# Optimization experiments

Hardware: AMD Instinct MI355X
Metric: run time of the kernel (lower is better)

Reference implementation:

```python
import jax, jax.numpy as jnp
import numpy as np

CDIM = 256  # part_size for energy_pooling_mask


def setup_inputs() -> dict:
    key = jax.random.key(0)
    ks = jax.random.split(key, 6)
    B, T, IDIM, HDIM, ODIM = 8, 2048, 512, 2048, 512
    x = jax.random.normal(ks[0], (B, T, IDIM), dtype=jnp.float32)
    mask_prev = jax.random.randint(ks[1], (B, T, HDIM), 0, 2, dtype=jnp.int32)
    W_enc = jax.random.normal(ks[2], (HDIM, IDIM), dtype=jnp.float32) * 0.02
    b_enc = jax.random.normal(ks[3], (HDIM,), dtype=jnp.float32) * 0.02
    W_dec = jax.random.normal(ks[4], (ODIM, HDIM), dtype=jnp.float32) * 0.02
    b_dec = jax.random.normal(ks[5], (ODIM,), dtype=jnp.float32) * 0.02
    return {"x": x, "mask_prev": mask_prev, "W_enc": W_enc, "b_enc": b_enc,
            "W_dec": W_dec, "b_dec": b_dec}


def _energy_pooling_mask(h, part_size):
    # topk over channel (last) dim of h^2; share=True -> k = 2*part_size
    B, T, H = h.shape
    k2 = 2 * part_size
    _, idx = jax.lax.top_k(h * h, k2)            # [B, T, 2c] unique indices
    idx_f = idx.reshape(B * T, k2)
    rows = jnp.arange(B * T)[:, None]
    base = jnp.zeros((B * T, H), dtype=h.dtype)
    # sum of one-hots over unique indices == scatter-set of 1.0
    mask_share = base.at[rows, idx_f].set(1.0).reshape(B, T, H)
    mask_cur = base.at[rows, idx_f[:, :part_size]].set(1.0).reshape(B, T, H)
    return mask_cur, mask_share


def reference(x, mask_prev, W_enc, b_enc, W_dec, b_dec):
    # encoder: Linear(idim -> hdim)
    h = jnp.einsum('bti,hi->bth', x, W_enc) + b_enc
    # hidden_exclude_activation with mask_prev given:
    # h[mask_prev.bool()] = 0
    mp = mask_prev.astype(h.dtype)
    h = jnp.where(mp > 0, jnp.zeros((), h.dtype), h)
    mask_cur, mask_cur_share = _energy_pooling_mask(h, CDIM)
    mask_prev_new = mp + mask_cur
    # h.masked_fill(~mask_cur_share.bool(), 0)
    h = h * mask_cur_share
    # decoder_src: Linear(hdim -> odim)
    out = jnp.einsum('bth,oh->bto', h, W_dec) + b_dec
    return out, mask_prev_new
```

## Files before the change

### kernel.cpp

```cpp
#include <hip/hip_runtime.h>
#include <hip/hip_bf16.h>

typedef __attribute__((ext_vector_type(8))) __bf16 bf16x8;
typedef __attribute__((ext_vector_type(4))) float f32x4;

#define MDIM 16384
#define HDIM 2048
#define IDIM 512
#define ODIM 512
#define SCAP 512

static __device__ __forceinline__ unsigned short f2bf(float f) {
  unsigned int u = __float_as_uint(f);
  unsigned int r = (u + 0x7fffu + ((u >> 16) & 1u)) >> 16;
  return (unsigned short)r;
}

__global__ void cvt_bf16_kernel(const float* __restrict__ src,
                                unsigned short* __restrict__ dst, int n) {
  int i = (blockIdx.x * 256 + threadIdx.x) * 4;
  if (i >= n) return;
  float4 v = *(const float4*)(src + i);
  unsigned int a = (unsigned int)f2bf(v.x) | ((unsigned int)f2bf(v.y) << 16);
  unsigned int b = (unsigned int)f2bf(v.z) | ((unsigned int)f2bf(v.w) << 16);
  uint2 st; st.x = a; st.y = b;
  *(uint2*)(dst + i) = st;
}

__global__ __launch_bounds__(256) void gemm1_kernel(
    const float* __restrict__ x,
    const float* __restrict__ wenc,
    const float* __restrict__ benc,
    float* __restrict__ h) {
  __shared__ __align__(16) float As[32][132];
  __shared__ __align__(16) float Bs[32][132];
  const int t = threadIdx.x;
  const int tx = t & 15, ty = t >> 4;
  const int m0 = blockIdx.y * 128;
  const int n0 = blockIdx.x * 128;
  const int r0 = t >> 1;
  const int kh = (t & 1) * 16;

  const float* pa = x + (size_t)(m0 + r0) * IDIM + kh;
  const float* pb = wenc + (size_t)(n0 + r0) * IDIM + kh;

  float acc[8][8];
#pragma unroll
  for (int i = 0; i < 8; ++i)
#pragma unroll
    for (int j = 0; j < 8; ++j) acc[i][j] = 0.f;

  for (int kt = 0; kt < IDIM; kt += 32) {
    float4 a0 = *(const float4*)(pa + kt);
    float4 a1 = *(const float4*)(pa + kt + 4);
    float4 a2 = *(const float4*)(pa + kt + 8);
    float4 a3 = *(const float4*)(pa + kt + 12);
    float4 b0 = *(const float4*)(pb + kt);
    float4 b1 = *(const float4*)(pb + kt + 4);
    float4 b2 = *(const float4*)(pb + kt + 8);
    float4 b3 = *(const float4*)(pb + kt + 12);
    __syncthreads();
    {
      const float av[16] = {a0.x, a0.y, a0.z, a0.w, a1.x, a1.y, a1.z, a1.w,
                            a2.x, a2.y, a2.z, a2.w, a3.x, a3.y, a3.z, a3.w};
      const float bv[16] = {b0.x, b0.y, b0.z, b0.w, b1.x, b1.y, b1.z, b1.w,
                            b2.x, b2.y, b2.z, b2.w, b3.x, b3.y, b3.z, b3.w};
#pragma unroll
      for (int j = 0; j < 16; ++j) {
        As[kh + j][r0] = av[j];
        Bs[kh + j][r0] = bv[j];
      }
    }
    __syncthreads();
#pragma unroll
    for (int k = 0; k < 32; ++k) {
      float4 av0 = *(const float4*)&As[k][ty * 4];
      float4 av1 = *(const float4*)&As[k][64 + ty * 4];
      float4 bv0 = *(const float4*)&Bs[k][tx * 4];
      float4 bv1 = *(const float4*)&Bs[k][64 + tx * 4];
      float am[8] = {av0.x, av0.y, av0.z, av0.w, av1.x, av1.y, av1.z, av1.w};
      float bm[8] = {bv0.x, bv0.y, bv0.z, bv0.w, bv1.x, bv1.y, bv1.z, bv1.w};
#pragma unroll
      for (int i = 0; i < 8; ++i)
#pragma unroll
        for (int j = 0; j < 8; ++j) acc[i][j] += am[i] * bm[j];
    }
  }
  float4 be0 = *(const float4*)(benc + n0 + tx * 4);
  float4 be1 = *(const float4*)(benc + n0 + 64 + tx * 4);
  float bb[8] = {be0.x, be0.y, be0.z, be0.w, be1.x, be1.y, be1.z, be1.w};
#pragma unroll
  for (int i = 0; i < 8; ++i) {
    int m = m0 + ((i < 4) ? (ty * 4 + i) : (64 + ty * 4 + (i - 4)));
    float* hrow = h + (size_t)m * HDIM + n0;
    float4 s0 = {acc[i][0] + bb[0], acc[i][1] + bb[1], acc[i][2] + bb[2], acc[i][3] + bb[3]};
    float4 s1 = {acc[i][4] + bb[4], acc[i][5] + bb[5], acc[i][6] + bb[6], acc[i][7] + bb[7]};
    *(float4*)(hrow + tx * 4) = s0;
    *(float4*)(hrow + 64 + tx * 4) = s1;
  }
}

__global__ __launch_bounds__(256, 4) void select_kernel(
    float* __restrict__ hbuf,
    const int* __restrict__ maskp,
    unsigned short* __restrict__ hs) {
  const int t = threadIdx.x;
  const int lane = t & 63;
  const int w = t >> 6;
  const int row = blockIdx.x * 4 + w;

  __shared__ int hist[4][1024];
  __shared__ unsigned int cand[4][2][SCAP];
  __shared__ int nc[4][2];

  int* H = hist[w];
  float* hrow = hbuf + (size_t)row * HDIM;
  const int* mrow = maskp + (size_t)row * HDIM;
  unsigned short* hsrow = hs + (size_t)row * HDIM;

  {
    int4 z = {0, 0, 0, 0};
#pragma unroll
    for (int i = 0; i < 4; ++i) *(int4*)&H[(i * 64 + lane) * 4] = z;
  }
  if (lane == 0) { nc[w][0] = 0; nc[w][1] = 0; }

  unsigned int key[8][4];
  uint2 hvb[8];
  unsigned int mmbits = 0;
#pragma unroll
  for (int s = 0; s < 8; ++s) {
    float4 hv = *(const float4*)(hrow + (s * 64 + lane) * 4);
    int4 mv = *(const int4*)(mrow + (s * 64 + lane) * 4);
    float h0 = (mv.x > 0) ? 0.f : hv.x;
    float h1 = (mv.y > 0) ? 0.f : hv.y;
    float h2 = (mv.z > 0) ? 0.f : hv.z;
    float h3 = (mv.w > 0) ? 0.f : hv.w;
    mmbits |= ((mv.x > 0) ? 1u : 0u) << (s * 4 + 0);
    mmbits |= ((mv.y > 0) ? 1u : 0u) << (s * 4 + 1);
    mmbits |= ((mv.z > 0) ? 1u : 0u) << (s * 4 + 2);
    mmbits |= ((mv.w > 0) ? 1u : 0u) << (s * 4 + 3);
    key[s][0] = __float_as_uint(h0 * h0);
    key[s][1] = __float_as_uint(h1 * h1);
    key[s][2] = __float_as_uint(h2 * h2);
    key[s][3] = __float_as_uint(h3 * h3);
    hvb[s].x = (unsigned int)f2bf(h0) | ((unsigned int)f2bf(h1) << 16);
    hvb[s].y = (unsigned int)f2bf(h2) | ((unsigned int)f2bf(h3) << 16);
  }

#pragma unroll
  for (int s = 0; s < 8; ++s)
#pragma unroll
    for (int c = 0; c < 4; ++c)
      if (key[s][c]) atomicAdd(&H[key[s][c] >> 21], 1);

  int q[16];
#pragma unroll
  for (int i = 0; i < 16; i += 4) {
    int4 hh = *(const int4*)&H[lane * 16 + i];
    q[i] = hh.x; q[i + 1] = hh.y; q[i + 2] = hh.z; q[i + 3] = hh.w;
  }
  int ls = 0;
#pragma unroll
  for (int i = 0; i < 16; ++i) ls += q[i];
  int rs = ls;
#pragma unroll
  for (int d = 1; d < 64; d <<= 1) {
    int o = __shfl_down(rs, d, 64);
    rs += (lane + d < 64) ? o : 0;
  }
  int f512 = -1, f256 = -1;
  {
    int c = rs - ls;
#pragma unroll
    for (int i = 15; i >= 0; --i) {
      int hc = q[i];
      if (c < 512 && c + hc >= 512) f512 = ((lane * 16 + i) << 12) | (512 - c);
      if (c < 256 && c + hc >= 256) f256 = ((lane * 16 + i) << 12) | (256 - c);
      c += hc;
    }
  }
#pragma unroll
  for (int d = 1; d < 64; d <<= 1) {
    f512 = max(f512, __shfl_xor(f512, d, 64));
    f256 = max(f256, __shfl_xor(f256, d, 64));
  }
  int b512, rb512, b256, rb256;
  if (f512 < 0) { b512 = 0; rb512 = 0x40000000; } else { b512 = f512 >> 12; rb512 = f512 & 0xfff; }
  if (f256 < 0) { b256 = 0; rb256 = 0x40000000; } else { b256 = f256 >> 12; rb256 = f256 & 0xfff; }

  unsigned int* c5 = cand[w][0];
  unsigned int* c2 = cand[w][1];
#pragma unroll
  for (int s = 0; s < 8; ++s)
#pragma unroll
    for (int c = 0; c < 4; ++c) {
      unsigned int k = key[s][c];
      if (k) {
        int bin = (int)(k >> 21);
        if (bin == b512) { int p = atomicAdd(&nc[w][0], 1); if (p < SCAP) c5[p] = k; }
        if (bin == b256) { int p = atomicAdd(&nc[w][1], 1); if (p < SCAP) c2[p] = k; }
      }
    }
  int C5 = nc[w][0]; C5 = (C5 < SCAP) ? C5 : SCAP;
  int C2 = nc[w][1]; C2 = (C2 < SCAP) ? C2 : SCAP;

  const int half = lane >> 5;
  const int hl = lane & 31;
  unsigned int bb = half ? (unsigned int)b256 : (unsigned int)b512;
  int rr = half ? rb256 : rb512;
  const unsigned int* cd = half ? c2 : c5;
  int C = half ? C2 : C5;
  unsigned int v = 0;
  if (rr <= C) {
    v = bb << 21;
    for (int bit = 20; bit >= 0; --bit) {
      unsigned int cth = v | (1u << bit);
      int cnt = 0;
      for (int p = hl; p < C; p += 32) cnt += (cd[p] >= cth) ? 1 : 0;
#pragma unroll
      for (int d = 1; d < 32; d <<= 1) cnt += __shfl_xor(cnt, d, 64);
      if (cnt >= rr) v = cth;
    }
  }
  const unsigned int v512 = (unsigned int)__shfl((int)v, 0, 64);
  const unsigned int v256 = (unsigned int)__shfl((int)v, 32, 64);

  int g = 0;
#pragma unroll
  for (int s = 0; s < 8; ++s)
#pragma unroll
    for (int c = 0; c < 4; ++c) {
      g += (key[s][c] > v512) ? 1 : 0;
      g += (key[s][c] > v256) ? (1 << 16) : 0;
    }
#pragma unroll
  for (int d = 1; d < 64; d <<= 1) g += __shfl_xor(g, d, 64);
  const int rg512 = 512 - (g & 0xffff);
  const int rg256 = 256 - (g >> 16);

  int excl = 0;
#pragma unroll
  for (int s = 0; s < 8; ++s) {
    int tcnt = 0;
#pragma unroll
    for (int c = 0; c < 4; ++c) {
      tcnt += (key[s][c] == v512) ? 1 : 0;
      tcnt += (key[s][c] == v256) ? (1 << 16) : 0;
    }
    int incl = tcnt;
#pragma unroll
    for (int d = 1; d < 64; d <<= 1) {
      int o = __shfl_up(incl, d, 64);
      if (lane >= d) incl += o;
    }
    int myexcl = excl + incl - tcnt;
    int tot = __shfl(incl, 63, 64);
    int run512 = myexcl & 0xffff;
    int run256 = (myexcl >> 16) & 0xffff;
    float mpn[4];
    unsigned int hb0 = hvb[s].x, hb1 = hvb[s].y;
#pragma unroll
    for (int c = 0; c < 4; ++c) {
      unsigned int k = key[s][c];
      bool share, cur;
      if (k > v512) share = true;
      else if (k == v512) { share = (run512 < rg512); run512++; }
      else share = false;
      if (k > v256) cur = true;
      else if (k == v256) { cur = (run256 < rg256); run256++; }
      else cur = false;
      int mm = (mmbits >> (s * 4 + c)) & 1;
      mpn[c] = (float)mm + (cur ? 1.0f : 0.0f);
      if (!share) {
        if (c == 0) hb0 &= 0xffff0000u;
        if (c == 1) hb0 &= 0x0000ffffu;
        if (c == 2) hb1 &= 0xffff0000u;
        if (c == 3) hb1 &= 0x0000ffffu;
      }
    }
    float4 so = {mpn[0], mpn[1], mpn[2], mpn[3]};
    *(float4*)(hrow + (s * 64 + lane) * 4) = so;
    uint2 ho = {hb0, hb1};
    *(uint2*)(hsrow + (s * 64 + lane) * 4) = ho;
    excl += tot;
  }
}

__global__ __launch_bounds__(256) void gemm2_kernel(
    const unsigned short* __restrict__ A,
    const unsigned short* __restrict__ B,
    const float* __restrict__ bdec,
    float* __restrict__ out) {
  __shared__ __align__(16) unsigned short As[64 * 40];
  __shared__ __align__(16) unsigned short Bs[128 * 40];
  const int t = threadIdx.x;
  const int lane = t & 63;
  const int w = t >> 6;
  const int wm = w >> 1, wn = w & 1;
  const int m0 = blockIdx.y * 64;
  const int n0 = blockIdx.x * 128;
  const int r = t >> 2;
  const int k8 = (t & 3) * 8;

  f32x4 acc[2][4];
#pragma unroll
  for (int i = 0; i < 2; ++i)
#pragma unroll
    for (int j = 0; j < 4; ++j) acc[i][j] = (f32x4){0.f, 0.f, 0.f, 0.f};

  const int la = lane & 15;
  const int kq = (lane >> 4) * 8;

  const unsigned short* pa = A + (size_t)(m0 + r) * HDIM + k8;
  const unsigned short* pb0 = B + (size_t)(n0 + r) * HDIM + k8;
  const unsigned short* pb1 = B + (size_t)(n0 + 64 + r) * HDIM + k8;

  uint4 a0 = *(const uint4*)(pa);
  uint4 b0 = *(const uint4*)(pb0);
  uint4 b1 = *(const uint4*)(pb1);

  for (int kt = 0; kt < HDIM; kt += 32) {
    __syncthreads();
    *(uint4*)&As[r * 40 + k8] = a0;
    *(uint4*)&Bs[r * 40 + k8] = b0;
    *(uint4*)&Bs[(64 + r) * 40 + k8] = b1;
    __syncthreads();
    if (kt + 32 < HDIM) {
      a0 = *(const uint4*)(pa + kt + 32);
      b0 = *(const uint4*)(pb0 + kt + 32);
      b1 = *(const uint4*)(pb1 + kt + 32);
    }
    bf16x8 af[2], bg[4];
#pragma unroll
    for (int mi = 0; mi < 2; ++mi)
      af[mi] = *(const bf16x8*)&As[(wm * 32 + mi * 16 + la) * 40 + kq];
#pragma unroll
    for (int ni = 0; ni < 4; ++ni)
      bg[ni] = *(const bf16x8*)&Bs[(wn * 64 + ni * 16 + la) * 40 + kq];
#pragma unroll
    for (int mi = 0; mi < 2; ++mi)
#pragma unroll
      for (int ni = 0; ni < 4; ++ni)
        acc[mi][ni] = __builtin_amdgcn_mfma_f32_16x16x32_bf16(
            af[mi], bg[ni], acc[mi][ni], 0, 0, 0);
  }
  const int rq = (lane >> 4) * 4;
#pragma unroll
  for (int mi = 0; mi < 2; ++mi) {
#pragma unroll
    for (int ni = 0; ni < 4; ++ni) {
      int n = n0 + wn * 64 + ni * 16 + la;
      float bd = bdec[n];
#pragma unroll
      for (int rr = 0; rr < 4; ++rr) {
        int m = m0 + wm * 32 + mi * 16 + rq + rr;
        out[(size_t)m * ODIM + n] = acc[mi][ni][rr] + bd;
      }
    }
  }
}

extern "C" void kernel_launch(void* const* d_in, const int* in_sizes, int n_in,
                              void* d_out, int out_size, void* d_ws, size_t ws_size,
                              hipStream_t stream) {
  const float* x = (const float*)d_in[0];
  const int* mask_prev = (const int*)d_in[1];
  const float* W_enc = (const float*)d_in[2];
  const float* b_enc = (const float*)d_in[3];
  const float* W_dec = (const float*)d_in[4];
  const float* b_dec = (const float*)d_in[5];

  float* out = (float*)d_out;
  float* hbuf = out + (size_t)MDIM * ODIM;
  unsigned short* hs = (unsigned short*)d_ws;
  unsigned short* wdec = hs + (size_t)MDIM * HDIM;

  cvt_bf16_kernel<<<dim3((ODIM * HDIM) / (256 * 4)), dim3(256), 0, stream>>>(
      W_dec, wdec, ODIM * HDIM);
  gemm1_kernel<<<dim3(HDIM / 128, MDIM / 128), dim3(256), 0, stream>>>(
      x, W_enc, b_enc, hbuf);
  select_kernel<<<dim3(MDIM / 4), dim3(256), 0, stream>>>(hbuf, mask_prev, hs);
  gemm2_kernel<<<dim3(ODIM / 128, MDIM / 64), dim3(256), 0, stream>>>(
      hs, wdec, b_dec, out);
}
```

Baseline: 752.9 us.

## Fuse W_dec bf16 conversion into gemm2 and add tie-free fast path in select

Drops the separate kernel that converts W_dec to bf16; gemm2 now loads fp32 W_dec and packs it to bf16 while staging into shared memory, removing one launch and an intermediate buffer. In the select kernel, the first few candidate values are cached in registers for the radix-threshold search, and when the tie counts match exactly the remaining slots, a fast path replaces the per-segment prefix-scan tie-breaking. The cost is that gemm2 now reads twice the bytes for B tiles and spends extra ALU on conversion in every block, since W_dec is reconverted per M-tile.

```diff
diff --git a/kernel.cpp b/kernel.cpp
--- a/kernel.cpp
+++ b/kernel.cpp
@@ -16,15 +16,13 @@
   return (unsigned short)r;
 }
 
-__global__ void cvt_bf16_kernel(const float* __restrict__ src,
-                                unsigned short* __restrict__ dst, int n) {
-  int i = (blockIdx.x * 256 + threadIdx.x) * 4;
-  if (i >= n) return;
-  float4 v = *(const float4*)(src + i);
-  unsigned int a = (unsigned int)f2bf(v.x) | ((unsigned int)f2bf(v.y) << 16);
-  unsigned int b = (unsigned int)f2bf(v.z) | ((unsigned int)f2bf(v.w) << 16);
-  uint2 st; st.x = a; st.y = b;
-  *(uint2*)(dst + i) = st;
+static __device__ __forceinline__ uint4 pack8bf(float4 x, float4 y) {
+  uint4 o;
+  o.x = (unsigned int)f2bf(x.x) | ((unsigned int)f2bf(x.y) << 16);
+  o.y = (unsigned int)f2bf(x.z) | ((unsigned int)f2bf(x.w) << 16);
+  o.z = (unsigned int)f2bf(y.x) | ((unsigned int)f2bf(y.y) << 16);
+  o.w = (unsigned int)f2bf(y.z) | ((unsigned int)f2bf(y.w) << 16);
+  return o;
 }
 
 __global__ __launch_bounds__(256) void gemm1_kernel(
@@ -213,11 +211,16 @@
   int C = half ? C2 : C5;
   unsigned int v = 0;
   if (rr <= C) {
+    unsigned int rc0 = (hl < C) ? cd[hl] : 0u;
+    unsigned int rc1 = (hl + 32 < C) ? cd[hl + 32] : 0u;
+    unsigned int rc2 = (hl + 64 < C) ? cd[hl + 64] : 0u;
+    unsigned int rc3 = (hl + 96 < C) ? cd[hl + 96] : 0u;
     v = bb << 21;
     for (int bit = 20; bit >= 0; --bit) {
       unsigned int cth = v | (1u << bit);
-      int cnt = 0;
-      for (int p = hl; p < C; p += 32) cnt += (cd[p] >= cth) ? 1 : 0;
+      int cnt = ((rc0 >= cth) ? 1 : 0) + ((rc1 >= cth) ? 1 : 0) +
+                ((rc2 >= cth) ? 1 : 0) + ((rc3 >= cth) ? 1 : 0);
+      for (int p = hl + 128; p < C; p += 32) cnt += (cd[p] >= cth) ? 1 : 0;
 #pragma unroll
       for (int d = 1; d < 32; d <<= 1) cnt += __shfl_xor(cnt, d, 64);
       if (cnt >= rr) v = cth;
@@ -226,70 +229,103 @@
   const unsigned int v512 = (unsigned int)__shfl((int)v, 0, 64);
   const unsigned int v256 = (unsigned int)__shfl((int)v, 32, 64);
 
-  int g = 0;
+  int g = 0, e = 0;
 #pragma unroll
   for (int s = 0; s < 8; ++s)
 #pragma unroll
     for (int c = 0; c < 4; ++c) {
       g += (key[s][c] > v512) ? 1 : 0;
       g += (key[s][c] > v256) ? (1 << 16) : 0;
-    }
-#pragma unroll
-  for (int d = 1; d < 64; d <<= 1) g += __shfl_xor(g, d, 64);
+      e += (key[s][c] == v512) ? 1 : 0;
+      e += (key[s][c] == v256) ? (1 << 16) : 0;
+    }
+#pragma unroll
+  for (int d = 1; d < 64; d <<= 1) {
+    g += __shfl_xor(g, d, 64);
+    e += __shfl_xor(e, d, 64);
+  }
   const int rg512 = 512 - (g & 0xffff);
   const int rg256 = 256 - (g >> 16);
-
-  int excl = 0;
-#pragma unroll
-  for (int s = 0; s < 8; ++s) {
-    int tcnt = 0;
-#pragma unroll
-    for (int c = 0; c < 4; ++c) {
-      tcnt += (key[s][c] == v512) ? 1 : 0;
-      tcnt += (key[s][c] == v256) ? (1 << 16) : 0;
-    }
-    int incl = tcnt;
-#pragma unroll
-    for (int d = 1; d < 64; d <<= 1) {
-      int o = __shfl_up(incl, d, 64);
-      if (lane >= d) incl += o;
-    }
-    int myexcl = excl + incl - tcnt;
-    int tot = __shfl(incl, 63, 64);
-    int run512 = myexcl & 0xffff;
-    int run256 = (myexcl >> 16) & 0xffff;
-    float mpn[4];
-    unsigned int hb0 = hvb[s].x, hb1 = hvb[s].y;
-#pragma unroll
-    for (int c = 0; c < 4; ++c) {
-      unsigned int k = key[s][c];
-      bool share, cur;
-      if (k > v512) share = true;
-      else if (k == v512) { share = (run512 < rg512); run512++; }
-      else share = false;
-      if (k > v256) cur = true;
-      else if (k == v256) { cur = (run256 < rg256); run256++; }
-      else cur = false;
-      int mm = (mmbits >> (s * 4 + c)) & 1;
-      mpn[c] = (float)mm + (cur ? 1.0f : 0.0f);
-      if (!share) {
-        if (c == 0) hb0 &= 0xffff0000u;
-        if (c == 1) hb0 &= 0x0000ffffu;
-        if (c == 2) hb1 &= 0xffff0000u;
-        if (c == 3) hb1 &= 0x0000ffffu;
-      }
-    }
-    float4 so = {mpn[0], mpn[1], mpn[2], mpn[3]};
-    *(float4*)(hrow + (s * 64 + lane) * 4) = so;
-    uint2 ho = {hb0, hb1};
-    *(uint2*)(hsrow + (s * 64 + lane) * 4) = ho;
-    excl += tot;
+  const int e512 = e & 0xffff;
+  const int e256 = e >> 16;
+
+  if (e512 == rg512 && e256 == rg256) {
+#pragma unroll
+    for (int s = 0; s < 8; ++s) {
+      float mpn[4];
+      unsigned int hb0 = hvb[s].x, hb1 = hvb[s].y;
+#pragma unroll
+      for (int c = 0; c < 4; ++c) {
+        unsigned int k = key[s][c];
+        bool share = (k >= v512);
+        bool cur = (k >= v256);
+        int mm = (mmbits >> (s * 4 + c)) & 1;
+        mpn[c] = (float)mm + (cur ? 1.0f : 0.0f);
+        if (!share) {
+          if (c == 0) hb0 &= 0xffff0000u;
+          if (c == 1) hb0 &= 0x0000ffffu;
+          if (c == 2) hb1 &= 0xffff0000u;
+          if (c == 3) hb1 &= 0x0000ffffu;
+        }
+      }
+      float4 so = {mpn[0], mpn[1], mpn[2], mpn[3]};
+      *(float4*)(hrow + (s * 64 + lane) * 4) = so;
+      uint2 ho = {hb0, hb1};
+      *(uint2*)(hsrow + (s * 64 + lane) * 4) = ho;
+    }
+  } else {
+    int excl = 0;
+#pragma unroll
+    for (int s = 0; s < 8; ++s) {
+      int tcnt = 0;
+#pragma unroll
+      for (int c = 0; c < 4; ++c) {
+        tcnt += (key[s][c] == v512) ? 1 : 0;
+        tcnt += (key[s][c] == v256) ? (1 << 16) : 0;
+      }
+      int incl = tcnt;
+#pragma unroll
+      for (int d = 1; d < 64; d <<= 1) {
+        int o = __shfl_up(incl, d, 64);
+        if (lane >= d) incl += o;
+      }
+      int myexcl = excl + incl - tcnt;
+      int tot = __shfl(incl, 63, 64);
+      int run512 = myexcl & 0xffff;
+      int run256 = (myexcl >> 16) & 0xffff;
+      float mpn[4];
+      unsigned int hb0 = hvb[s].x, hb1 = hvb[s].y;
+#pragma unroll
+      for (int c = 0; c < 4; ++c) {
+        unsigned int k = key[s][c];
+        bool share, cur;
+        if (k > v512) share = true;
+        else if (k == v512) { share = (run512 < rg512); run512++; }
+        else share = false;
+        if (k > v256) cur = true;
+        else if (k == v256) { cur = (run256 < rg256); run256++; }
+        else cur = false;
+        int mm = (mmbits >> (s * 4 + c)) & 1;
+        mpn[c] = (float)mm + (cur ? 1.0f : 0.0f);
+        if (!share) {
+          if (c == 0) hb0 &= 0xffff0000u;
+          if (c == 1) hb0 &= 0x0000ffffu;
+          if (c == 2) hb1 &= 0xffff0000u;
+          if (c == 3) hb1 &= 0x0000ffffu;
+        }
+      }
+      float4 so = {mpn[0], mpn[1], mpn[2], mpn[3]};
+      *(float4*)(hrow + (s * 64 + lane) * 4) = so;
+      uint2 ho = {hb0, hb1};
+      *(uint2*)(hsrow + (s * 64 + lane) * 4) = ho;
+      excl += tot;
+    }
   }
 }
 
 __global__ __launch_bounds__(256) void gemm2_kernel(
     const unsigned short* __restrict__ A,
-    const unsigned short* __restrict__ B,
+    const float* __restrict__ Wd,
     const float* __restrict__ bdec,
     float* __restrict__ out) {
   __shared__ __align__(16) unsigned short As[64 * 40];
@@ -313,23 +349,27 @@
   const int kq = (lane >> 4) * 8;
 
   const unsigned short* pa = A + (size_t)(m0 + r) * HDIM + k8;
-  const unsigned short* pb0 = B + (size_t)(n0 + r) * HDIM + k8;
-  const unsigned short* pb1 = B + (size_t)(n0 + 64 + r) * HDIM + k8;
+  const float* pb0 = Wd + (size_t)(n0 + r) * HDIM + k8;
+  const float* pb1 = Wd + (size_t)(n0 + 64 + r) * HDIM + k8;
 
   uint4 a0 = *(const uint4*)(pa);
-  uint4 b0 = *(const uint4*)(pb0);
-  uint4 b1 = *(const uint4*)(pb1);
+  float4 b0a = *(const float4*)(pb0);
+  float4 b0b = *(const float4*)(pb0 + 4);
+  float4 b1a = *(const float4*)(pb1);
+  float4 b1b = *(const float4*)(pb1 + 4);
 
   for (int kt = 0; kt < HDIM; kt += 32) {
     __syncthreads();
     *(uint4*)&As[r * 40 + k8] = a0;
-    *(uint4*)&Bs[r * 40 + k8] = b0;
-    *(uint4*)&Bs[(64 + r) * 40 + k8] = b1;
+    *(uint4*)&Bs[r * 40 + k8] = pack8bf(b0a, b0b);
+    *(uint4*)&Bs[(64 + r) * 40 + k8] = pack8bf(b1a, b1b);
     __syncthreads();
     if (kt + 32 < HDIM) {
       a0 = *(const uint4*)(pa + kt + 32);
-      b0 = *(const uint4*)(pb0 + kt + 32);
-      b1 = *(const uint4*)(pb1 + kt + 32);
+      b0a = *(const float4*)(pb0 + kt + 32);
+      b0b = *(const float4*)(pb0 + kt + 36);
+      b1a = *(const float4*)(pb1 + kt + 32);
+      b1b = *(const float4*)(pb1 + kt + 36);
     }
     bf16x8 af[2], bg[4];
 #pragma unroll
@@ -374,13 +414,10 @@
   float* out = (float*)d_out;
   float* hbuf = out + (size_t)MDIM * ODIM;
   unsigned short* hs = (unsigned short*)d_ws;
-  unsigned short* wdec = hs + (size_t)MDIM * HDIM;
-
-  cvt_bf16_kernel<<<dim3((ODIM * HDIM) / (256 * 4)), dim3(256), 0, stream>>>(
-      W_dec, wdec, ODIM * HDIM);
+
   gemm1_kernel<<<dim3(HDIM / 128, MDIM / 128), dim3(256), 0, stream>>>(
       x, W_enc, b_enc, hbuf);
   select_kernel<<<dim3(MDIM / 4), dim3(256), 0, stream>>>(hbuf, mask_prev, hs);
   gemm2_kernel<<<dim3(ODIM / 128, MDIM / 64), dim3(256), 0, stream>>>(
-      hs, wdec, b_dec, out);
-}
+      hs, W_dec, b_dec, out);
+}
```

After: 755.0 us. No clear change (+0.3%).
